# Kernel optimization log

Hardware: AMD Instinct MI355X
Metric: run time of the kernel (lower is better)

Reference implementation:

```python
import jax, jax.numpy as jnp
import numpy as np
from jax import lax

B = 16
DEPTH = 24
D_MODEL = 192
D_INNER = 384   # expand=2
D_STATE = 16
D_CONV = 4
DT_RANK = 12    # ceil(192/16)
PATCH = 16
EPS = 1e-5


def setup_inputs() -> dict:
    key = jax.random.key(0)
    ks = jax.random.split(key, 24)
    def n(k, shape, s):
        return jax.random.normal(k, shape, jnp.float32) * s
    inp = {}
    inp["x_img"] = jax.random.normal(ks[0], (B, 3, 256, 256), jnp.float32)
    inp["z_img"] = jax.random.normal(ks[1], (B, 3, 128, 128), jnp.float32)
    # patch embed conv
    inp["patch_w"] = n(ks[2], (D_MODEL, 3, PATCH, PATCH), 0.02)
    inp["patch_b"] = jnp.zeros((D_MODEL,), jnp.float32)
    # abs pos embeds (token counts fixed by module: 256 for x, 64 for z)
    inp["pos_x"] = n(ks[3], (1, 256, D_MODEL), 0.02)
    inp["pos_z"] = n(ks[4], (1, 64, D_MODEL), 0.02)
    # per-layer norms (LayerNorm, rms_norm=False)
    inp["ln_w"] = jnp.ones((DEPTH, D_MODEL), jnp.float32)
    inp["ln_b"] = jnp.zeros((DEPTH, D_MODEL), jnp.float32)
    # Mamba mixer params (stacked over depth)
    inp["in_w"] = n(ks[5], (DEPTH, 2 * D_INNER, D_MODEL), 0.05)          # in_proj (no bias)
    inp["conv_w"] = n(ks[6], (DEPTH, D_INNER, D_CONV), 0.2)              # depthwise conv1d
    inp["conv_b"] = jnp.zeros((DEPTH, D_INNER), jnp.float32)
    inp["xproj_w"] = n(ks[7], (DEPTH, DT_RANK + 2 * D_STATE, D_INNER), 0.05)  # x_proj (no bias)
    inp["dt_w"] = n(ks[8], (DEPTH, D_INNER, DT_RANK), 0.1)               # dt_proj weight
    # dt bias ~ inverse-softplus of dt in [1e-3, 0.1] (Mamba init)
    dt = jnp.exp(jax.random.uniform(ks[9], (DEPTH, D_INNER)) * (np.log(0.1) - np.log(1e-3)) + np.log(1e-3))
    inp["dt_b"] = dt + jnp.log(-jnp.expm1(-dt))
    # A_log init: log(1..d_state) per channel
    inp["A_log"] = jnp.log(jnp.tile(jnp.arange(1, D_STATE + 1, dtype=jnp.float32), (DEPTH, D_INNER, 1)))
    inp["D_skip"] = jnp.ones((DEPTH, D_INNER), jnp.float32)
    inp["out_w"] = n(ks[10], (DEPTH, D_MODEL, D_INNER), 0.05)            # out_proj (no bias)
    inp["fnorm_w"] = jnp.ones((D_MODEL,), jnp.float32)
    inp["fnorm_b"] = jnp.zeros((D_MODEL,), jnp.float32)
    return inp


def _layer_norm(x, w, b):
    mu = jnp.mean(x, axis=-1, keepdims=True)
    var = jnp.mean(jnp.square(x - mu), axis=-1, keepdims=True)
    return (x - mu) * lax.rsqrt(var + EPS) * w + b


def _patch_embed(img, w, b):
    # Conv2d stride=patch, then flatten HW -> tokens
    y = lax.conv_general_dilated(img, w, (PATCH, PATCH), 'VALID',
                                 dimension_numbers=('NCHW', 'OIHW', 'NCHW'))
    y = y + b[None, :, None, None]
    Bn, D, H, W = y.shape
    return y.reshape(Bn, D, H * W).transpose(0, 2, 1)  # (B, HW, D)


def _ssm_scan(dA, dBu):
    # h_t = dA_t * h_{t-1} + dBu_t, parallel over time via associative scan
    def comb(e1, e2):
        a1, b1 = e1
        a2, b2 = e2
        return a2 * a1, a2 * b1 + b2
    _, h = lax.associative_scan(comb, (dA, dBu), axis=1)
    return h  # (B, L, D_INNER, D_STATE)


def _mamba(h, in_w, conv_w, conv_b, xproj_w, dt_w, dt_b, A_log, D_skip, out_w):
    # h: (B, L, D_MODEL)
    xz = h @ in_w.T                                   # (B, L, 2*D_INNER)
    xc, zg = jnp.split(xz, 2, axis=-1)
    # causal depthwise conv over time
    xt = xc.transpose(0, 2, 1)                        # (B, D_INNER, L)
    xt = lax.conv_general_dilated(xt, conv_w[:, None, :], (1,), [(D_CONV - 1, 0)],
                                  feature_group_count=D_INNER,
                                  dimension_numbers=('NCH', 'OIH', 'NCH'))
    xt = xt + conv_b[None, :, None]
    xc = jax.nn.silu(xt).transpose(0, 2, 1)           # (B, L, D_INNER)
    dbl = xc @ xproj_w.T                              # (B, L, dt_rank + 2*d_state)
    dt, Bm, Cm = jnp.split(dbl, [DT_RANK, DT_RANK + D_STATE], axis=-1)
    dt = jax.nn.softplus(dt @ dt_w.T + dt_b)          # (B, L, D_INNER)
    A = -jnp.exp(A_log)                               # (D_INNER, D_STATE)
    dA = jnp.exp(dt[..., None] * A)                   # (B, L, D_INNER, D_STATE)
    dBu = dt[..., None] * Bm[:, :, None, :] * xc[..., None]
    hs = _ssm_scan(dA, dBu)
    y = jnp.einsum('bldn,bln->bld', hs, Cm) + xc * D_skip
    y = y * jax.nn.silu(zg)
    return y @ out_w.T                                # (B, L, D_MODEL)


def reference(x_img, z_img, patch_w, patch_b, pos_x, pos_z, ln_w, ln_b,
              in_w, conv_w, conv_b, xproj_w, dt_w, dt_b, A_log, D_skip,
              out_w, fnorm_w, fnorm_b):
    x_tok = _patch_embed(x_img, patch_w, patch_b) + pos_x   # (B, 256, D)
    z_tok = _patch_embed(z_img, patch_w, patch_b) + pos_z   # (B, 64, D)
    hidden = jnp.concatenate([z_tok, x_tok], axis=1)        # (B, 320, D)
    residual = None
    for i in range(DEPTH):
        # fused add-norm prenorm: residual = hidden + residual; hidden = LN(residual)
        residual = hidden if residual is None else hidden + residual
        h_n = _layer_norm(residual, ln_w[i], ln_b[i])
        hidden = _mamba(h_n, in_w[i], conv_w[i], conv_b[i], xproj_w[i],
                        dt_w[i], dt_b[i], A_log[i], D_skip[i], out_w[i])
    residual = residual + hidden
    return _layer_norm(residual, fnorm_w, fnorm_b)          # (B, 320, D), final_pool_type='none'
```

## Files before the change

kernel.cpp:

```cpp
#include <hip/hip_runtime.h>
#include <hip/hip_bf16.h>

#define BB 16
#define DEPTH 24
#define DM 192
#define DI 384
#define DS 16
#define DC 4
#define DTR 12
#define LL 320
#define NX 256
#define NZ 64
#define NT (BB * LL)
#define NC 10
#define LC 32
#define EPSV 1e-5f

__device__ inline float siluf(float x) { return x / (1.f + __expf(-x)); }
__device__ inline float softplusf(float x) {
    return (x > 20.f) ? x : log1pf(expf(x));
}
__device__ inline float wave_sum64(float v) {
    #pragma unroll
    for (int o = 32; o > 0; o >>= 1) v += __shfl_xor(v, o);
    return v;
}

__global__ void zero_kernel(float* p, int n) {
    int i = blockIdx.x * blockDim.x + threadIdx.x;
    if (i < n) p[i] = 0.f;
}

__global__ __launch_bounds__(256) void addnorm_kernel(const float* hidden,
                                                      float* __restrict__ residual,
                                                      float* hn,
                                                      const float* __restrict__ w,
                                                      const float* __restrict__ bias,
                                                      size_t off) {
    int t = blockIdx.x * 4 + (threadIdx.x >> 6);
    int lane = threadIdx.x & 63;
    size_t base = (size_t)t * DM;
    float a = residual[base + lane]       + hidden[base + lane];
    float b = residual[base + 64 + lane]  + hidden[base + 64 + lane];
    float c = residual[base + 128 + lane] + hidden[base + 128 + lane];
    residual[base + lane] = a;
    residual[base + 64 + lane] = b;
    residual[base + 128 + lane] = c;
    float mu = wave_sum64(a + b + c) * (1.f / 192.f);
    float va = a - mu, vb = b - mu, vc = c - mu;
    float var = wave_sum64(va * va + vb * vb + vc * vc) * (1.f / 192.f);
    float inv = rsqrtf(var + EPSV);
    hn[base + lane]       = va * inv * w[off + lane]       + bias[off + lane];
    hn[base + 64 + lane]  = vb * inv * w[off + 64 + lane]  + bias[off + 64 + lane];
    hn[base + 128 + lane] = vc * inv * w[off + 128 + lane] + bias[off + 128 + lane];
}

template<int K, int KT, int NO>
__global__ __launch_bounds__(256) void gemm_rt(const float* __restrict__ x,
                                               const float* __restrict__ w,
                                               size_t woff,
                                               float* __restrict__ out, int N) {
    constexpr int NCOL = 64 * NO;
    constexpr int KC = KT / 4;
    __shared__ float xs[32][KT + 4];
    __shared__ float ws[NCOL][KT + 4];
    int t0 = blockIdx.x * 32;
    int j0 = blockIdx.y * NCOL;
    int lane = threadIdx.x & 63;
    int wv = threadIdx.x >> 6;
    float acc[8][NO];
    #pragma unroll
    for (int t = 0; t < 8; t++)
        #pragma unroll
        for (int o = 0; o < NO; o++) acc[t][o] = 0.f;

    for (int kt = 0; kt < K; kt += KT) {
        for (int idx = threadIdx.x; idx < 32 * KC; idx += 256) {
            int tt = idx / KC, kc = idx % KC;
            float4 v = *(const float4*)&x[(size_t)(t0 + tt) * K + kt + kc * 4];
            *(float4*)&xs[tt][kc * 4] = v;
        }
        for (int idx = threadIdx.x; idx < NCOL * KC; idx += 256) {
            int jj = idx / KC, kc = idx % KC;
            float4 v = *(const float4*)&w[woff + (size_t)(j0 + jj) * K + kt + kc * 4];
            *(float4*)&ws[jj][kc * 4] = v;
        }
        __syncthreads();
        #pragma unroll 2
        for (int kk = 0; kk < KT; kk += 4) {
            float4 xv[8];
            #pragma unroll
            for (int t = 0; t < 8; t++)
                xv[t] = *(const float4*)&xs[wv * 8 + t][kk];
            #pragma unroll
            for (int o = 0; o < NO; o++) {
                float4 wv4 = *(const float4*)&ws[lane + 64 * o][kk];
                #pragma unroll
                for (int t = 0; t < 8; t++)
                    acc[t][o] += xv[t].x * wv4.x + xv[t].y * wv4.y
                               + xv[t].z * wv4.z + xv[t].w * wv4.w;
            }
        }
        __syncthreads();
    }
    #pragma unroll
    for (int t = 0; t < 8; t++)
        #pragma unroll
        for (int o = 0; o < NO; o++)
            out[(size_t)(t0 + wv * 8 + t) * N + j0 + lane + 64 * o] = acc[t][o];
}

__global__ __launch_bounds__(256) void patch_rt(const float* __restrict__ img,
                                                const float* __restrict__ w,
                                                const float* __restrict__ bias,
                                                const float* __restrict__ pos,
                                                float* __restrict__ hidden,
                                                int side, int tok_off) {
    __shared__ float xs[32][100];
    __shared__ float ws[64][100];
    int ntok = side * side;
    int pt0 = blockIdx.x * 32;
    int j0 = blockIdx.y * 64;
    int S = side * 16;
    int lane = threadIdx.x & 63;
    int wv = threadIdx.x >> 6;
    float acc[8];
    #pragma unroll
    for (int t = 0; t < 8; t++) acc[t] = 0.f;

    for (int kt = 0; kt < 768; kt += 96) {
        for (int idx = threadIdx.x; idx < 32 * 24; idx += 256) {
            int tt = idx / 24, kc = idx % 24;
            int k = kt + kc * 4;
            int c = k >> 8, p = k & 255, pi = p >> 4, pj = p & 15;
            int patch = pt0 + tt;
            int b = patch / ntok, t = patch % ntok;
            int ph = t / side, pw = t % side;
            float4 v = *(const float4*)&img[((size_t)(b * 3 + c) * S + ph * 16 + pi) * S
                                            + pw * 16 + pj];
            *(float4*)&xs[tt][kc * 4] = v;
        }
        for (int idx = threadIdx.x; idx < 64 * 24; idx += 256) {
            int jj = idx / 24, kc = idx % 24;
            float4 v = *(const float4*)&w[(size_t)(j0 + jj) * 768 + kt + kc * 4];
            *(float4*)&ws[jj][kc * 4] = v;
        }
        __syncthreads();
        #pragma unroll 2
        for (int kk = 0; kk < 96; kk += 4) {
            float4 xv[8];
            #pragma unroll
            for (int t = 0; t < 8; t++)
                xv[t] = *(const float4*)&xs[wv * 8 + t][kk];
            float4 wv4 = *(const float4*)&ws[lane][kk];
            #pragma unroll
            for (int t = 0; t < 8; t++)
                acc[t] += xv[t].x * wv4.x + xv[t].y * wv4.y
                        + xv[t].z * wv4.z + xv[t].w * wv4.w;
        }
        __syncthreads();
    }
    float bj = bias[j0 + lane];
    #pragma unroll
    for (int t = 0; t < 8; t++) {
        int patch = pt0 + wv * 8 + t;
        int b = patch / ntok, tk = patch % ntok;
        hidden[((size_t)b * LL + tok_off + tk) * DM + j0 + lane] =
            acc[t] + bj + pos[(size_t)tk * DM + j0 + lane];
    }
}

__global__ __launch_bounds__(256) void xpd_kernel(const float* __restrict__ xz,
                                                  const float* __restrict__ cw,
                                                  const float* __restrict__ cb,
                                                  const float* __restrict__ xpw,
                                                  const float* __restrict__ dtw,
                                                  const float* __restrict__ dtbias,
                                                  float* __restrict__ xc,
                                                  float* __restrict__ dbl,
                                                  float* __restrict__ dtbuf,
                                                  int layer) {
    __shared__ float smem[5760];
    float* xs   = smem;
    float* ws   = smem + 832;
    float* sdbl = smem;
    float* sdtw = smem + 768;

    int t0 = blockIdx.x * 16;
    int l0 = t0 % LL;
    int lane = threadIdx.x & 63;
    int wv = threadIdx.x >> 6;
    const float* cwl = cw  + (size_t)layer * DI * DC;
    const float* cbl = cb  + (size_t)layer * DI;
    const float* xpl = xpw + (size_t)layer * 44 * DI;
    float acc[4] = {0.f, 0.f, 0.f, 0.f};

    for (int kt = 0; kt < DI; kt += 48) {
        for (int idx = threadIdx.x; idx < 16 * 48; idx += 256) {
            int tt = idx / 48, kk = idx % 48;
            int d = kt + kk;
            float a = cbl[d];
            #pragma unroll
            for (int r = 0; r < 4; r++) {
                int l = l0 + tt - 3 + r;
                float v = (l >= 0) ? xz[(size_t)(t0 + tt - 3 + r) * 768 + d] : 0.f;
                a += cwl[d * 4 + r] * v;
            }
            a = siluf(a);
            xs[tt * 52 + kk] = a;
            xc[(size_t)(t0 + tt) * DI + d] = a;
        }
        for (int idx = threadIdx.x; idx < 64 * 12; idx += 256) {
            int jj = idx / 12, kc = idx % 12;
            float4 v = make_float4(0.f, 0.f, 0.f, 0.f);
            if (jj < 44)
                v = *(const float4*)&xpl[(size_t)jj * DI + kt + kc * 4];
            *(float4*)&ws[jj * 52 + kc * 4] = v;
        }
        __syncthreads();
        const float* wr0 = ws + lane * 52;
        #pragma unroll 4
        for (int kk = 0; kk < 48; kk += 4) {
            float4 xv0 = *(const float4*)&xs[(wv * 4 + 0) * 52 + kk];
            float4 xv1 = *(const float4*)&xs[(wv * 4 + 1) * 52 + kk];
            float4 xv2 = *(const float4*)&xs[(wv * 4 + 2) * 52 + kk];
            float4 xv3 = *(const float4*)&xs[(wv * 4 + 3) * 52 + kk];
            float4 wv4 = *(const float4*)&wr0[kk];
            acc[0] += xv0.x * wv4.x + xv0.y * wv4.y + xv0.z * wv4.z + xv0.w * wv4.w;
            acc[1] += xv1.x * wv4.x + xv1.y * wv4.y + xv1.z * wv4.z + xv1.w * wv4.w;
            acc[2] += xv2.x * wv4.x + xv2.y * wv4.y + xv2.z * wv4.z + xv2.w * wv4.w;
            acc[3] += xv3.x * wv4.x + xv3.y * wv4.y + xv3.z * wv4.z + xv3.w * wv4.w;
        }
        __syncthreads();
    }
    if (lane < 44) {
        #pragma unroll
        for (int t = 0; t < 4; t++) {
            sdbl[(wv * 4 + t) * 48 + lane] = acc[t];
            dbl[(size_t)(t0 + wv * 4 + t) * 44 + lane] = acc[t];
        }
    }
    const float* dwl = dtw + (size_t)layer * DI * DTR;
    for (int idx = threadIdx.x; idx < DI * DTR; idx += 256) {
        int d = idx / 12, r = idx % 12;
        sdtw[d * 13 + r] = dwl[idx];
    }
    __syncthreads();
    const float* dbb = dtbias + (size_t)layer * DI;
    for (int idx = threadIdx.x; idx < 16 * DI; idx += 256) {
        int tt = idx / DI, d = idx % DI;
        float a = dbb[d];
        const float* br = sdbl + tt * 48;
        const float* wr = sdtw + d * 13;
        #pragma unroll
        for (int r = 0; r < 12; r++) a += br[r] * wr[r];
        dtbuf[(size_t)(t0 + tt) * DI + d] = softplusf(a);
    }
}

__global__ __launch_bounds__(256) void scanA(const float* __restrict__ dt,
                                             const float* __restrict__ xc,
                                             const float* __restrict__ dbl,
                                             const float* __restrict__ A_log,
                                             float* __restrict__ Pout,
                                             float* __restrict__ Hout,
                                             size_t aoff) {
    int Q = blockIdx.x * 64 + (threadIdx.x >> 2);
    int n0 = threadIdx.x & 3;
    int d = Q % DI;
    int bc = Q / DI;
    int b = bc / NC, c = bc % NC;
    float4 Al = *(const float4*)&A_log[aoff + (size_t)d * DS + n0 * 4];
    float A0 = -expf(Al.x), A1 = -expf(Al.y), A2 = -expf(Al.z), A3 = -expf(Al.w);
    float h0 = 0.f, h1 = 0.f, h2 = 0.f, h3 = 0.f;
    float P0 = 1.f, P1 = 1.f, P2 = 1.f, P3 = 1.f;
    int tbase = b * LL + c * LC;
    for (int l = 0; l < LC; l++) {
        size_t t = (size_t)tbase + l;
        float dtv = dt[t * DI + d];
        float xcv = xc[t * DI + d];
        float4 B4 = *(const float4*)&dbl[t * 44 + DTR + n0 * 4];
        float s = dtv * xcv;
        float e0 = __expf(dtv * A0), e1 = __expf(dtv * A1);
        float e2 = __expf(dtv * A2), e3 = __expf(dtv * A3);
        h0 = e0 * h0 + s * B4.x;  P0 *= e0;
        h1 = e1 * h1 + s * B4.y;  P1 *= e1;
        h2 = e2 * h2 + s * B4.z;  P2 *= e2;
        h3 = e3 * h3 + s * B4.w;  P3 *= e3;
    }
    size_t gi = (size_t)Q * 16 + n0 * 4;
    *(float4*)&Pout[gi] = make_float4(P0, P1, P2, P3);
    *(float4*)&Hout[gi] = make_float4(h0, h1, h2, h3);
}

__global__ __launch_bounds__(256) void scanC(const float* __restrict__ dt,
                                             const float* xc,
                                             const float* __restrict__ dbl,
                                             const float* __restrict__ xz,
                                             const float* __restrict__ A_log,
                                             const float* __restrict__ Dskip,
                                             const float* __restrict__ Pin,
                                             const float* __restrict__ Hin,
                                             float* y,
                                             size_t aoff, size_t doff) {
    int Q = blockIdx.x * 64 + (threadIdx.x >> 2);
    int n0 = threadIdx.x & 3;
    int d = Q % DI;
    int bc = Q / DI;
    int b = bc / NC, c = bc % NC;
    float h0 = 0.f, h1 = 0.f, h2 = 0.f, h3 = 0.f;
    for (int cc = 0; cc < c; cc++) {
        size_t gi = ((size_t)(b * NC + cc) * DI + d) * 16 + n0 * 4;
        float4 P4 = *(const float4*)&Pin[gi];
        float4 H4 = *(const float4*)&Hin[gi];
        h0 = P4.x * h0 + H4.x;
        h1 = P4.y * h1 + H4.y;
        h2 = P4.z * h2 + H4.z;
        h3 = P4.w * h3 + H4.w;
    }
    float4 Al = *(const float4*)&A_log[aoff + (size_t)d * DS + n0 * 4];
    float A0 = -expf(Al.x), A1 = -expf(Al.y), A2 = -expf(Al.z), A3 = -expf(Al.w);
    float Dv = Dskip[doff + d];
    int tbase = b * LL + c * LC;
    for (int l = 0; l < LC; l++) {
        size_t t = (size_t)tbase + l;
        float dtv = dt[t * DI + d];
        float xcv = xc[t * DI + d];
        float4 B4 = *(const float4*)&dbl[t * 44 + DTR + n0 * 4];
        float4 C4 = *(const float4*)&dbl[t * 44 + DTR + DS + n0 * 4];
        float s = dtv * xcv;
        float e0 = __expf(dtv * A0), e1 = __expf(dtv * A1);
        float e2 = __expf(dtv * A2), e3 = __expf(dtv * A3);
        h0 = e0 * h0 + s * B4.x;
        h1 = e1 * h1 + s * B4.y;
        h2 = e2 * h2 + s * B4.z;
        h3 = e3 * h3 + s * B4.w;
        float p = h0 * C4.x + h1 * C4.y + h2 * C4.z + h3 * C4.w;
        p += __shfl_xor(p, 1);
        p += __shfl_xor(p, 2);
        if (n0 == 0) {
            float zg = xz[t * (2 * DI) + DI + d];
            y[t * DI + d] = (p + xcv * Dv) * siluf(zg);
        }
    }
}

__global__ __launch_bounds__(256) void final_kernel(const float* __restrict__ hidden,
                                                    const float* __restrict__ residual,
                                                    const float* __restrict__ w,
                                                    const float* __restrict__ bias,
                                                    float* __restrict__ out) {
    int t = blockIdx.x * 4 + (threadIdx.x >> 6);
    int lane = threadIdx.x & 63;
    size_t base = (size_t)t * DM;
    float a = residual[base + lane]       + hidden[base + lane];
    float b = residual[base + 64 + lane]  + hidden[base + 64 + lane];
    float c = residual[base + 128 + lane] + hidden[base + 128 + lane];
    float mu = wave_sum64(a + b + c) * (1.f / 192.f);
    float va = a - mu, vb = b - mu, vc = c - mu;
    float var = wave_sum64(va * va + vb * vb + vc * vc) * (1.f / 192.f);
    float inv = rsqrtf(var + EPSV);
    out[base + lane]       = va * inv * w[lane]       + bias[lane];
    out[base + 64 + lane]  = vb * inv * w[64 + lane]  + bias[64 + lane];
    out[base + 128 + lane] = vc * inv * w[128 + lane] + bias[128 + lane];
}

extern "C" void kernel_launch(void* const* d_in, const int* in_sizes, int n_in,
                              void* d_out, int out_size, void* d_ws, size_t ws_size,
                              hipStream_t stream) {
    const float* x_img   = (const float*)d_in[0];
    const float* z_img   = (const float*)d_in[1];
    const float* patch_w = (const float*)d_in[2];
    const float* patch_b = (const float*)d_in[3];
    const float* pos_x   = (const float*)d_in[4];
    const float* pos_z   = (const float*)d_in[5];
    const float* ln_w    = (const float*)d_in[6];
    const float* ln_b    = (const float*)d_in[7];
    const float* in_w    = (const float*)d_in[8];
    const float* conv_w  = (const float*)d_in[9];
    const float* conv_b  = (const float*)d_in[10];
    const float* xproj_w = (const float*)d_in[11];
    const float* dt_w    = (const float*)d_in[12];
    const float* dt_b    = (const float*)d_in[13];
    const float* A_log   = (const float*)d_in[14];
    const float* D_skip  = (const float*)d_in[15];
    const float* out_w   = (const float*)d_in[16];
    const float* fnorm_w = (const float*)d_in[17];
    const float* fnorm_b = (const float*)d_in[18];

    float* hidden   = (float*)d_ws;
    float* residual = hidden   + (size_t)NT * DM;
    float* xz       = residual + (size_t)NT * DM;
    float* xc       = xz       + (size_t)NT * 2 * DI;
    float* dbl      = xc       + (size_t)NT * DI;
    float* dtbuf    = dbl      + (size_t)NT * 44;
    float* scanP    = dtbuf    + (size_t)NT * DI;
    float* scanH    = scanP    + (size_t)BB * NC * DI * 16;
    float* hn       = hidden;
    float* yb       = xc;

    zero_kernel<<<(NT * DM + 255) / 256, 256, 0, stream>>>(residual, NT * DM);

    {
        dim3 gx(BB * NX / 32, 3), gz(BB * NZ / 32, 3);
        patch_rt<<<gx, 256, 0, stream>>>(x_img, patch_w, patch_b, pos_x,
                                         hidden, 16, NZ);
        patch_rt<<<gz, 256, 0, stream>>>(z_img, patch_w, patch_b, pos_z,
                                         hidden, 8, 0);
    }

    const int scan_blocks = BB * NC * DI / 64;
    for (int i = 0; i < DEPTH; i++) {
        addnorm_kernel<<<NT / 4, 256, 0, stream>>>(
            hidden, residual, hn, ln_w, ln_b, (size_t)i * DM);
        {
            dim3 g(NT / 32, 6);
            gemm_rt<192, 48, 2><<<g, 256, 0, stream>>>(
                hn, in_w, (size_t)i * 768 * 192, xz, 768);
        }
        xpd_kernel<<<NT / 16, 256, 0, stream>>>(
            xz, conv_w, conv_b, xproj_w, dt_w, dt_b, xc, dbl, dtbuf, i);
        scanA<<<scan_blocks, 256, 0, stream>>>(
            dtbuf, xc, dbl, A_log, scanP, scanH, (size_t)i * DI * DS);
        scanC<<<scan_blocks, 256, 0, stream>>>(
            dtbuf, xc, dbl, xz, A_log, D_skip, scanP, scanH, yb,
            (size_t)i * DI * DS, (size_t)i * DI);
        {
            dim3 g(NT / 32, 3);
            gemm_rt<384, 48, 1><<<g, 256, 0, stream>>>(
                yb, out_w, (size_t)i * 192 * 384, hidden, 192);
        }
    }

    final_kernel<<<NT / 4, 256, 0, stream>>>(hidden, residual, fnorm_w, fnorm_b,
                                             (float*)d_out);
}
```

Measured before the change: 4.217 ms.

## Fuse add+LayerNorm into in_proj GEMM, merge patch launches, ping-pong residual

Each in_proj GEMM block now computes the residual add and LayerNorm for its 32 tokens directly into shared memory. This removes the separate addnorm kernel and the round trip of the normalized activations through global memory. The residual is ping-ponged between the workspace and the output buffer, which removes the zero-fill kernel and the read-modify-write on the same buffer. The two patch-embed launches are merged into one grid, and the out_proj GEMM uses a larger K tile. The cost is that LayerNorm is recomputed in each of the six column blocks of a token tile.

Result: no change. 4.285 ms (+1.6%).

```diff
diff --git a/kernel.cpp b/kernel.cpp
--- a/kernel.cpp
+++ b/kernel.cpp
@@ -26,33 +26,83 @@
     return v;
 }
 
-__global__ void zero_kernel(float* p, int n) {
-    int i = blockIdx.x * blockDim.x + threadIdx.x;
-    if (i < n) p[i] = 0.f;
-}
-
-__global__ __launch_bounds__(256) void addnorm_kernel(const float* hidden,
-                                                      float* __restrict__ residual,
-                                                      float* hn,
-                                                      const float* __restrict__ w,
-                                                      const float* __restrict__ bias,
-                                                      size_t off) {
-    int t = blockIdx.x * 4 + (threadIdx.x >> 6);
+__global__ __launch_bounds__(256) void ln_gemm(const float* __restrict__ hidden,
+                                               const float* __restrict__ resin,
+                                               float* __restrict__ resout,
+                                               const float* __restrict__ lnw,
+                                               const float* __restrict__ lnb,
+                                               size_t lnoff,
+                                               const float* __restrict__ w,
+                                               size_t woff,
+                                               float* __restrict__ out,
+                                               int first) {
+    __shared__ float xs[32][196];
+    __shared__ float ws[128][52];
+    int t0 = blockIdx.x * 32;
+    int j0 = blockIdx.y * 128;
+    {
+        int tt = threadIdx.x >> 3;
+        int l8 = threadIdx.x & 7;
+        size_t base = (size_t)(t0 + tt) * DM;
+        float v[24];
+        float s = 0.f;
+        #pragma unroll
+        for (int j = 0; j < 24; j++) {
+            int e = l8 + 8 * j;
+            float x = hidden[base + e];
+            if (!first) x += resin[base + e];
+            v[j] = x;
+            s += x;
+        }
+        s += __shfl_xor(s, 1); s += __shfl_xor(s, 2); s += __shfl_xor(s, 4);
+        float mu = s * (1.f / 192.f);
+        float q = 0.f;
+        #pragma unroll
+        for (int j = 0; j < 24; j++) { float d = v[j] - mu; q += d * d; }
+        q += __shfl_xor(q, 1); q += __shfl_xor(q, 2); q += __shfl_xor(q, 4);
+        float inv = rsqrtf(q * (1.f / 192.f) + EPSV);
+        #pragma unroll
+        for (int j = 0; j < 24; j++) {
+            int e = l8 + 8 * j;
+            if (blockIdx.y == 0) resout[base + e] = v[j];
+            xs[tt][e] = (v[j] - mu) * inv * lnw[lnoff + e] + lnb[lnoff + e];
+        }
+    }
+    __syncthreads();
     int lane = threadIdx.x & 63;
-    size_t base = (size_t)t * DM;
-    float a = residual[base + lane]       + hidden[base + lane];
-    float b = residual[base + 64 + lane]  + hidden[base + 64 + lane];
-    float c = residual[base + 128 + lane] + hidden[base + 128 + lane];
-    residual[base + lane] = a;
-    residual[base + 64 + lane] = b;
-    residual[base + 128 + lane] = c;
-    float mu = wave_sum64(a + b + c) * (1.f / 192.f);
-    float va = a - mu, vb = b - mu, vc = c - mu;
-    float var = wave_sum64(va * va + vb * vb + vc * vc) * (1.f / 192.f);
-    float inv = rsqrtf(var + EPSV);
-    hn[base + lane]       = va * inv * w[off + lane]       + bias[off + lane];
-    hn[base + 64 + lane]  = vb * inv * w[off + 64 + lane]  + bias[off + 64 + lane];
-    hn[base + 128 + lane] = vc * inv * w[off + 128 + lane] + bias[off + 128 + lane];
+    int wv = threadIdx.x >> 6;
+    float acc[8][2];
+    #pragma unroll
+    for (int t = 0; t < 8; t++) { acc[t][0] = 0.f; acc[t][1] = 0.f; }
+    for (int kt = 0; kt < 192; kt += 48) {
+        for (int idx = threadIdx.x; idx < 128 * 12; idx += 256) {
+            int jj = idx / 12, kc = idx % 12;
+            float4 v4 = *(const float4*)&w[woff + (size_t)(j0 + jj) * 192 + kt + kc * 4];
+            *(float4*)&ws[jj][kc * 4] = v4;
+        }
+        __syncthreads();
+        #pragma unroll 2
+        for (int kk = 0; kk < 48; kk += 4) {
+            float4 xv[8];
+            #pragma unroll
+            for (int t = 0; t < 8; t++)
+                xv[t] = *(const float4*)&xs[wv * 8 + t][kt + kk];
+            #pragma unroll
+            for (int o = 0; o < 2; o++) {
+                float4 wv4 = *(const float4*)&ws[lane + 64 * o][kk];
+                #pragma unroll
+                for (int t = 0; t < 8; t++)
+                    acc[t][o] += xv[t].x * wv4.x + xv[t].y * wv4.y
+                               + xv[t].z * wv4.z + xv[t].w * wv4.w;
+            }
+        }
+        __syncthreads();
+    }
+    #pragma unroll
+    for (int t = 0; t < 8; t++)
+        #pragma unroll
+        for (int o = 0; o < 2; o++)
+            out[(size_t)(t0 + wv * 8 + t) * 768 + j0 + lane + 64 * o] = acc[t][o];
 }
 
 template<int K, int KT, int NO>
@@ -110,16 +160,22 @@
             out[(size_t)(t0 + wv * 8 + t) * N + j0 + lane + 64 * o] = acc[t][o];
 }
 
-__global__ __launch_bounds__(256) void patch_rt(const float* __restrict__ img,
+__global__ __launch_bounds__(256) void patch_rt(const float* __restrict__ x_img,
+                                                const float* __restrict__ z_img,
                                                 const float* __restrict__ w,
                                                 const float* __restrict__ bias,
-                                                const float* __restrict__ pos,
-                                                float* __restrict__ hidden,
-                                                int side, int tok_off) {
+                                                const float* __restrict__ pos_x,
+                                                const float* __restrict__ pos_z,
+                                                float* __restrict__ hidden) {
     __shared__ float xs[32][100];
     __shared__ float ws[64][100];
+    bool isx = blockIdx.x < (BB * NX / 32);
+    const float* img = isx ? x_img : z_img;
+    const float* pos = isx ? pos_x : pos_z;
+    int side = isx ? 16 : 8;
+    int tok_off = isx ? NZ : 0;
     int ntok = side * side;
-    int pt0 = blockIdx.x * 32;
+    int pt0 = (isx ? blockIdx.x : blockIdx.x - BB * NX / 32) * 32;
     int j0 = blockIdx.y * 64;
     int S = side * 16;
     int lane = threadIdx.x & 63;
@@ -396,27 +452,24 @@
     float* dtbuf    = dbl      + (size_t)NT * 44;
     float* scanP    = dtbuf    + (size_t)NT * DI;
     float* scanH    = scanP    + (size_t)BB * NC * DI * 16;
-    float* hn       = hidden;
     float* yb       = xc;
-
-    zero_kernel<<<(NT * DM + 255) / 256, 256, 0, stream>>>(residual, NT * DM);
+    float* resalt   = (float*)d_out;
 
     {
-        dim3 gx(BB * NX / 32, 3), gz(BB * NZ / 32, 3);
-        patch_rt<<<gx, 256, 0, stream>>>(x_img, patch_w, patch_b, pos_x,
-                                         hidden, 16, NZ);
-        patch_rt<<<gz, 256, 0, stream>>>(z_img, patch_w, patch_b, pos_z,
-                                         hidden, 8, 0);
+        dim3 gp((BB * NX + BB * NZ) / 32, 3);
+        patch_rt<<<gp, 256, 0, stream>>>(x_img, z_img, patch_w, patch_b,
+                                         pos_x, pos_z, hidden);
     }
 
     const int scan_blocks = BB * NC * DI / 64;
     for (int i = 0; i < DEPTH; i++) {
-        addnorm_kernel<<<NT / 4, 256, 0, stream>>>(
-            hidden, residual, hn, ln_w, ln_b, (size_t)i * DM);
+        const float* resin = (i % 2) ? resalt : residual;
+        float* resout      = (i % 2) ? residual : resalt;
         {
             dim3 g(NT / 32, 6);
-            gemm_rt<192, 48, 2><<<g, 256, 0, stream>>>(
-                hn, in_w, (size_t)i * 768 * 192, xz, 768);
+            ln_gemm<<<g, 256, 0, stream>>>(
+                hidden, resin, resout, ln_w, ln_b, (size_t)i * DM,
+                in_w, (size_t)i * 768 * 192, xz, i == 0 ? 1 : 0);
         }
         xpd_kernel<<<NT / 16, 256, 0, stream>>>(
             xz, conv_w, conv_b, xproj_w, dt_w, dt_b, xc, dbl, dtbuf, i);
@@ -427,7 +480,7 @@
             (size_t)i * DI * DS, (size_t)i * DI);
         {
             dim3 g(NT / 32, 3);
-            gemm_rt<384, 48, 1><<<g, 256, 0, stream>>>(
+            gemm_rt<384, 96, 1><<<g, 256, 0, stream>>>(
                 yb, out_w, (size_t)i * 192 * 384, hidden, 192);
         }
     }
```
